# Kernel optimization log

Hardware: AMD Instinct MI355X
Metric: run time of the kernel (lower is better)

## Reference

```python
import jax, jax.numpy as jnp
import numpy as np

EPS = 1e-5
NUM_HEADS = 8

def _bn(x, w, b, m, v):
    # inference-mode BatchNorm2d over channel dim of (B,C,H,W)
    inv = w / jnp.sqrt(v + EPS)
    return x * inv[None, :, None, None] + (b - m * inv)[None, :, None, None]

def _conv1x1(x, W, b):
    # 1x1 conv == per-pixel matmul: W is (out_ch, in_ch)
    return jnp.einsum('bchw,ec->behw', x, W) + b[None, :, None, None]

def _forward(x, bn1_w, bn1_b, bn1_m, bn1_v, Wq, bq, Wk, bk, Wv, bv, gamma, temperature,
             conv_w, conv_b, cbn_w, cbn_b, cbn_m, cbn_v, rs_w, rs_b, rbn_w, rbn_b, rbn_m, rbn_v):
    B, C, Wd, Hd = x.shape
    S = Wd * Hd
    E = Wq.shape[0]
    hd = E // NUM_HEADS
    xa = jax.nn.relu(_bn(x, bn1_w, bn1_b, bn1_m, bn1_v))
    def proj(Wm, bm):
        return _conv1x1(xa, Wm, bm).reshape(B, NUM_HEADS, hd, S).transpose(0, 1, 3, 2)  # (B,h,S,d)
    q = proj(Wq, bq)
    k = proj(Wk, bk)
    v = proj(Wv, bv)
    scores = jnp.einsum('bhsd,bhtd->bhst', q, k) / temperature  # (B,h,S,S)
    scores = scores - jnp.max(scores, axis=-1, keepdims=True)   # redundant amax-subtract as in source
    attn = jax.nn.softmax(scores, axis=-1)
    out = jnp.einsum('bhst,bhtd->bhsd', attn, v)
    out = out.transpose(0, 1, 3, 2).reshape(B, E, Wd, Hd)
    conv_path = jax.nn.relu(_bn(_conv1x1(x, conv_w, conv_b), cbn_w, cbn_b, cbn_m, cbn_v))
    fused = gamma[0] * out + conv_path
    return jax.nn.gelu(_bn(_conv1x1(fused, rs_w, rs_b), rbn_w, rbn_b, rbn_m, rbn_v), approximate=False)

def setup_inputs() -> dict:
    key = jax.random.key(0)
    ks = jax.random.split(key, 18)
    C, E = 256, 512
    n = lambda k, s, sc=0.02: jax.random.normal(k, s, jnp.float32) * sc
    return {
        'x': jax.random.normal(ks[0], (1, C, 64, 64), jnp.float32),
        'bn1_w': 1.0 + n(ks[1], (C,), 0.1), 'bn1_b': n(ks[2], (C,), 0.1),
        'bn1_m': n(ks[3], (C,), 0.05), 'bn1_v': 0.5 + jax.random.uniform(ks[4], (C,), jnp.float32),
        'Wq': n(ks[5], (E, C)), 'bq': jnp.zeros((E,), jnp.float32),
        'Wk': n(ks[6], (E, C)), 'bk': jnp.zeros((E,), jnp.float32),
        'Wv': n(ks[7], (E, C)), 'bv': jnp.zeros((E,), jnp.float32),
        'gamma': jnp.full((1,), 0.5, jnp.float32),
        'temperature': jnp.asarray(0.85, jnp.float32),
        'conv_w': n(ks[8], (E, C)), 'conv_b': jnp.zeros((E,), jnp.float32),
        'cbn_w': 1.0 + n(ks[9], (E,), 0.1), 'cbn_b': n(ks[10], (E,), 0.1),
        'cbn_m': n(ks[11], (E,), 0.05), 'cbn_v': 0.5 + jax.random.uniform(ks[12], (E,), jnp.float32),
        'rs_w': n(ks[13], (C, E)), 'rs_b': jnp.zeros((C,), jnp.float32),
        'rbn_w': 1.0 + n(ks[14], (C,), 0.1), 'rbn_b': n(ks[15], (C,), 0.1),
        'rbn_m': n(ks[16], (C,), 0.05), 'rbn_v': 0.5 + jax.random.uniform(ks[17], (C,), jnp.float32),
    }

def reference(x, bn1_w, bn1_b, bn1_m, bn1_v, Wq, bq, Wk, bk, Wv, bv, gamma, temperature,
              conv_w, conv_b, cbn_w, cbn_b, cbn_m, cbn_v, rs_w, rs_b, rbn_w, rbn_b, rbn_m, rbn_v):
    return _forward(x, bn1_w, bn1_b, bn1_m, bn1_v, Wq, bq, Wk, bk, Wv, bv, gamma, temperature,
                    conv_w, conv_b, cbn_w, cbn_b, cbn_m, cbn_v, rs_w, rs_b, rbn_w, rbn_b, rbn_m, rbn_v)
```

## Files before the change

kernel.cpp:

```cpp
#include <hip/hip_runtime.h>

#define S_DIM 4096
#define C_IN  256
#define E_DIM 512
#define HD    64
#define EPSV  1e-5f

typedef __attribute__((ext_vector_type(8))) short s8v;
typedef __attribute__((ext_vector_type(4))) short s4v;
typedef __attribute__((ext_vector_type(4))) float f4v;
typedef __attribute__((ext_vector_type(16))) float f16v;

__device__ __forceinline__ float bf2f(unsigned short h){
  union{unsigned u; float f;} v; v.u = ((unsigned)h)<<16; return v.f;
}
__device__ __forceinline__ unsigned short f2bf(float f){
  union{float f; unsigned u;} v; v.f = f;
  unsigned r = v.u + 0x7fffu + ((v.u>>16)&1u);
  return (unsigned short)(r>>16);
}
__device__ __forceinline__ unsigned cvtpk_bf16(float lo, float hi_){
  unsigned r;
  asm("v_cvt_pk_bf16_f32 %0, %1, %2" : "=v"(r) : "v"(lo), "v"(hi_));
  return r;
}
__device__ __forceinline__ s8v lds_rd8(const unsigned short* b, int row, int ck){
  return *(const s8v*)&b[(row<<6) + (((ck)^(row&7))<<3)];
}
__device__ __forceinline__ s4v lds_rd4q(const unsigned short* b, int row, int q4){
  return *(const s4v*)&b[(row<<6) + (((q4)^(row&15))<<2)];
}
__device__ __forceinline__ int swz64(int col, int row){
  return (col & ~56) | ((((col>>3)&7) ^ (row&7))<<3);
}
__device__ __forceinline__ void gl_lds16(const unsigned short* g, unsigned short* l){
  __builtin_amdgcn_global_load_lds(
      (const __attribute__((address_space(1))) unsigned int*)g,
      (__attribute__((address_space(3))) unsigned int*)l, 16, 0, 0);
}

__global__ __launch_bounds__(256) void k_pre(const float* __restrict__ w0,
    const float* __restrict__ w1, const float* __restrict__ w2,
    const float* __restrict__ w3, const float* __restrict__ w4,
    unsigned short* __restrict__ dst,
    const float* __restrict__ x,
    const float* __restrict__ bw, const float* __restrict__ bb,
    const float* __restrict__ bm, const float* __restrict__ bvar,
    unsigned short* __restrict__ XaT, unsigned short* __restrict__ XrT){
  int fb = blockIdx.x;
  int tid = threadIdx.x;
  if(fb < 2560){
    int z = fb >> 9, i = (fb & 511)*256 + tid;
    const float* s = (z==0)?w0:(z==1)?w1:(z==2)?w2:(z==3)?w3:w4;
    float v = s[i];
    int idx;
    if(z < 4){
      int e = i>>8, c = i&255;
      idx = z*(E_DIM*C_IN) + e*C_IN + swz64(c, e);
    } else {
      int c = i>>9, e = i&511;
      idx = 4*(E_DIM*C_IN) + c*E_DIM + swz64(e, c);
    }
    dst[idx] = f2bf(v);
    return;
  }
  int b = fb - 2560;
  __shared__ float tile[32][33];
  int tx = tid & 31, ty = tid >> 5;
  int s0 = (b & 127)*32, c0 = (b >> 7)*32;
  #pragma unroll
  for(int p=0;p<4;p++){
    int c = c0 + ty + p*8;
    tile[ty+p*8][tx] = x[c*S_DIM + s0 + tx];
  }
  __syncthreads();
  int cc = c0 + tx;
  float inv  = bw[cc] * rsqrtf(bvar[cc] + EPSV);
  float beta = bb[cc] - bm[cc]*inv;
  #pragma unroll
  for(int p=0;p<4;p++){
    int s = s0 + ty + p*8;
    float v = tile[tx][ty+p*8];
    float a = v*inv + beta; a = a>0.f?a:0.f;
    int ccp = swz64(cc, s);
    XaT[s*C_IN + ccp] = f2bf(a);
    XrT[s*C_IN + ccp] = f2bf(v);
  }
}

__global__ __launch_bounds__(256) void k_proj(
    const unsigned short* __restrict__ XaT, const unsigned short* __restrict__ XrT,
    const unsigned short* __restrict__ Wb,
    const float* __restrict__ bq, const float* __restrict__ bk,
    const float* __restrict__ bvb, const float* __restrict__ bc,
    const float* __restrict__ cw, const float* __restrict__ cbb,
    const float* __restrict__ cm, const float* __restrict__ cvv,
    unsigned short* __restrict__ QT, unsigned short* __restrict__ KT,
    unsigned short* __restrict__ Vx, unsigned short* __restrict__ CT){
  int z = blockIdx.z;
  const unsigned short* Xin = (z==3) ? XrT : XaT;
  const unsigned short* W   = Wb + z*(E_DIM*C_IN);
  const float* bias = (z==0)?bq:(z==1)?bk:(z==2)?bvb:bc;

  __shared__ unsigned short Als[128*64];
  __shared__ unsigned short Bls[64*64];
  int tid = threadIdx.x;
  int w = tid>>6, l = tid&63, g = l>>4, c16 = l&15;
  int wr = w>>1, wc = w&1;
  int s0 = blockIdx.y*128, e0 = blockIdx.x*64;

  f4v acc[4][2];
  #pragma unroll
  for(int m=0;m<4;m++)
    #pragma unroll
    for(int n=0;n<2;n++) acc[m][n] = (f4v){0.f,0.f,0.f,0.f};

  for(int kk=0;kk<4;kk++){
    __syncthreads();
    #pragma unroll
    for(int p=0;p<4;p++){
      int flat = p*256 + tid, row = flat>>3, ch = flat&7;
      gl_lds16(&Xin[(s0+row)*C_IN + kk*64 + ch*8], Als + (p*256 + w*64)*8);
    }
    #pragma unroll
    for(int p=0;p<2;p++){
      int flat = p*256 + tid, row = flat>>3, ch = flat&7;
      gl_lds16(&W[(e0+row)*C_IN + kk*64 + ch*8], Bls + (p*256 + w*64)*8);
    }
    asm volatile("s_waitcnt vmcnt(0)" ::: "memory");
    __syncthreads();
    #pragma unroll
    for(int kb=0;kb<2;kb++){
      s8v bfr[2];
      #pragma unroll
      for(int n=0;n<2;n++) bfr[n] = lds_rd8(Bls, wc*32 + n*16 + c16, g + kb*4);
      #pragma unroll
      for(int m=0;m<4;m++){
        s8v af = lds_rd8(Als, wr*64 + m*16 + c16, g + kb*4);
        #pragma unroll
        for(int n=0;n<2;n++)
          acc[m][n] = __builtin_amdgcn_mfma_f32_16x16x32_bf16(af, bfr[n], acc[m][n], 0,0,0);
      }
    }
  }
  #pragma unroll
  for(int n=0;n<2;n++){
    int e = e0 + wc*32 + n*16 + c16;
    float bsv = bias[e];
    float cinv = 0.f, cbeta = 0.f;
    if(z==3){ cinv = cw[e]*rsqrtf(cvv[e]+EPSV); cbeta = cbb[e] - cm[e]*cinv; }
    #pragma unroll
    for(int m=0;m<4;m++){
      int sb = s0 + wr*64 + m*16 + g*4;
      if(z==2){
        s4v pk;
        #pragma unroll
        for(int i=0;i<4;i++) pk[i] = (short)f2bf(acc[m][n][i] + bsv);
        int sb2 = (sb & ~63) | ((((sb>>2)&15) ^ (e&15))<<2);
        *(s4v*)&Vx[e*S_DIM + sb2] = pk;
      } else {
        unsigned short* dst = (z==0)?QT:(z==1)?KT:CT;
        #pragma unroll
        for(int i=0;i<4;i++){
          float vv = acc[m][n][i] + bsv;
          if(z==3){ vv = vv*cinv + cbeta; vv = vv>0.f?vv:0.f; }
          int key = sb+i;
          int ee = e;
          if(z==1) ee = swz64(e, key);
          dst[key*E_DIM + ee] = f2bf(vv);
        }
      }
    }
  }
}

__global__ __launch_bounds__(512,2) void k_attn(
    const unsigned short* __restrict__ QT, const unsigned short* __restrict__ KT,
    const unsigned short* __restrict__ Vx, const unsigned short* __restrict__ CT,
    const float* __restrict__ gamma, const float* __restrict__ temp,
    unsigned short* __restrict__ fusedT){
  __shared__ unsigned short SM[65536];
  int tid = threadIdx.x;
  int w = tid>>6, l = tid&63, l31 = l&31, hi = l>>5;
  int qh = w>>2, kh = w&3;
  int bx = blockIdx.x;
  int h = bx&7;
  int q0b = (bx>>3)*128;
  float scl = 1.4426950408889634f / temp[0];

  #define STAGE(BUF, T) { \
    _Pragma("unroll") \
    for(int j=0;j<8;j++){ \
      int flat = (w*8+j)*64 + l; \
      int tile = flat>>9, gg = flat&511, row = gg>>3, ch = gg&7; \
      int khp = tile&3; \
      int sK = khp*1024 + (T)*64; \
      const unsigned short* src = (tile<4) \
        ? &KT[(sK+row)*E_DIM + h*HD + ch*8] \
        : &Vx[(h*HD+row)*S_DIM + sK + ch*8]; \
      gl_lds16(src, SM + (BUF)*32768 + (w*8+j)*512); \
    } }

  STAGE(0, 0);

  s8v qf[2][4];
  #pragma unroll
  for(int qg=0;qg<2;qg++){
    int q = q0b + qh*64 + qg*32 + l31;
    #pragma unroll
    for(int ks=0;ks<4;ks++){
      s8v r = *(const s8v*)&QT[q*E_DIM + h*HD + ks*16 + hi*8];
      #pragma unroll
      for(int j=0;j<8;j++) qf[qg][ks][j] = (short)f2bf(bf2f((unsigned short)r[j])*scl);
    }
  }

  f16v oacc[2][2];
  #pragma unroll
  for(int qg=0;qg<2;qg++)
    #pragma unroll
    for(int dt=0;dt<2;dt++)
      #pragma unroll
      for(int r=0;r<16;r++) oacc[qg][dt][r]=0.f;
  float lrun[2] = {0.f, 0.f};

  int buf = 0;
  #pragma unroll 1
  for(int t=0;t<16;t++){
    asm volatile("s_waitcnt vmcnt(0)" ::: "memory");
    __syncthreads();
    if(t<15) STAGE(buf^1, t+1);
    const unsigned short* Kb = SM + buf*32768 + kh*4096;
    const unsigned short* Vb = SM + buf*32768 + (4+kh)*4096;

    #pragma unroll
    for(int sub=0;sub<2;sub++){
      int kr = sub*32 + l31;
      s8v kf[4];
      #pragma unroll
      for(int ks=0;ks<4;ks++) kf[ks] = lds_rd8(Kb, kr, ks*2 + hi);

      union{ s8v v; unsigned u[4]; } pa[2][2];
      #pragma unroll
      for(int qg=0;qg<2;qg++){
        f16v d;
        #pragma unroll
        for(int r=0;r<16;r++) d[r]=0.f;
        __builtin_amdgcn_s_setprio(1);
        #pragma unroll
        for(int ks=0;ks<4;ks++)
          d = __builtin_amdgcn_mfma_f32_32x32x16_bf16(kf[ks], qf[qg][ks], d, 0,0,0);
        __builtin_amdgcn_s_setprio(0);
        float e_[16], ls = 0.f;
        #pragma unroll
        for(int r=0;r<16;r++){ e_[r] = __builtin_amdgcn_exp2f(d[r]); ls += e_[r]; }
        lrun[qg] += ls;
        #pragma unroll
        for(int j=0;j<4;j++){
          pa[qg][0].u[j] = cvtpk_bf16(e_[2*j],   e_[2*j+1]);
          pa[qg][1].u[j] = cvtpk_bf16(e_[8+2*j], e_[8+2*j+1]);
        }
      }
      __builtin_amdgcn_s_setprio(1);
      #pragma unroll
      for(int dt=0;dt<2;dt++){
        int vr = dt*32 + l31;
        union{ s8v v; s4v h2[2]; } vf;
        vf.h2[0] = lds_rd4q(Vb, vr, sub*8 + hi);
        vf.h2[1] = lds_rd4q(Vb, vr, sub*8 + 2 + hi);
        oacc[0][dt] = __builtin_amdgcn_mfma_f32_32x32x16_bf16(pa[0][0].v, vf.v, oacc[0][dt], 0,0,0);
        oacc[1][dt] = __builtin_amdgcn_mfma_f32_32x32x16_bf16(pa[1][0].v, vf.v, oacc[1][dt], 0,0,0);
        vf.h2[0] = lds_rd4q(Vb, vr, sub*8 + 4 + hi);
        vf.h2[1] = lds_rd4q(Vb, vr, sub*8 + 6 + hi);
        oacc[0][dt] = __builtin_amdgcn_mfma_f32_32x32x16_bf16(pa[0][1].v, vf.v, oacc[0][dt], 0,0,0);
        oacc[1][dt] = __builtin_amdgcn_mfma_f32_32x32x16_bf16(pa[1][1].v, vf.v, oacc[1][dt], 0,0,0);
      }
      __builtin_amdgcn_s_setprio(0);
    }
    buf ^= 1;
  }

  #pragma unroll
  for(int qg=0;qg<2;qg++) lrun[qg] += __shfl_xor(lrun[qg], 32);

  float* slab = (float*)SM;
  float* l_buf = slab + 6*64*33;
  float ga = gamma[0];
  #pragma unroll
  for(int qg=0;qg<2;qg++){
    __syncthreads();
    if(kh!=0){
      float* dst = slab + ((qh*3 + (kh-1))*64 + l)*33;
      #pragma unroll
      for(int r=0;r<16;r++){ dst[r] = oacc[qg][0][r]; dst[16+r] = oacc[qg][1][r]; }
      dst[32] = lrun[qg];
    }
    __syncthreads();
    if(kh==0){
      float lt = lrun[qg];
      #pragma unroll
      for(int s=0;s<3;s++){
        const float* src = slab + ((qh*3 + s)*64 + l)*33;
        #pragma unroll
        for(int r=0;r<16;r++){ oacc[qg][0][r] += src[r]; oacc[qg][1][r] += src[16+r]; }
        lt += src[32];
      }
      if(hi==0) l_buf[qh*32 + l31] = lt;
    }
    __syncthreads();
    if(kh==0){
      #pragma unroll
      for(int g4=0;g4<4;g4++){
        float4 lv = *(float4*)&l_buf[qh*32 + g4*8 + hi*4];
        float rl[4] = {ga/lv.x, ga/lv.y, ga/lv.z, ga/lv.w};
        #pragma unroll
        for(int dt=0;dt<2;dt++){
          int e = h*HD + dt*32 + l31;
          #pragma unroll
          for(int j=0;j<4;j++){
            int r = g4*4 + j;
            int qrow = q0b + qh*64 + qg*32 + j + g4*8 + hi*4;
            float o = oacc[qg][dt][r]*rl[j] + bf2f(CT[qrow*E_DIM + e]);
            fusedT[qrow*E_DIM + swz64(e, qrow)] = f2bf(o);
          }
        }
      }
    }
  }
  #undef STAGE
}

__global__ __launch_bounds__(256) void k_final(
    const unsigned short* __restrict__ Wrs,
    const unsigned short* __restrict__ fusedT,
    const float* __restrict__ rsb,
    const float* __restrict__ rw, const float* __restrict__ rbb,
    const float* __restrict__ rm, const float* __restrict__ rv,
    float* __restrict__ out){
  __shared__ unsigned short Als[64*64];
  __shared__ unsigned short Bls[64*64];
  int tid = threadIdx.x;
  int w = tid>>6, l = tid&63, g = l>>4, c16 = l&15;
  int wr2 = w>>1, wc2 = w&1;
  int sB0 = blockIdx.x*64, c0 = blockIdx.y*64;
  f4v acc[2][2];
  #pragma unroll
  for(int m=0;m<2;m++)
    #pragma unroll
    for(int n=0;n<2;n++) acc[m][n]=(f4v){0.f,0.f,0.f,0.f};
  for(int kk=0;kk<8;kk++){
    __syncthreads();
    #pragma unroll
    for(int p=0;p<2;p++){
      int flat = p*256+tid, row=flat>>3, ch=flat&7;
      gl_lds16(&Wrs[(c0+row)*E_DIM + kk*64 + ch*8], Als + (p*256 + w*64)*8);
    }
    #pragma unroll
    for(int p=0;p<2;p++){
      int flat = p*256+tid, row=flat>>3, ch=flat&7;
      gl_lds16(&fusedT[(sB0+row)*E_DIM + kk*64 + ch*8], Bls + (p*256 + w*64)*8);
    }
    asm volatile("s_waitcnt vmcnt(0)" ::: "memory");
    __syncthreads();
    #pragma unroll
    for(int kb=0;kb<2;kb++){
      s8v af[2]; s8v bfr[2];
      #pragma unroll
      for(int m=0;m<2;m++) af[m] = lds_rd8(Als, wr2*32 + m*16 + c16, g + kb*4);
      #pragma unroll
      for(int n=0;n<2;n++) bfr[n] = lds_rd8(Bls, wc2*32 + n*16 + c16, g + kb*4);
      #pragma unroll
      for(int m=0;m<2;m++)
        #pragma unroll
        for(int n=0;n<2;n++)
          acc[m][n] = __builtin_amdgcn_mfma_f32_16x16x32_bf16(af[m], bfr[n], acc[m][n],0,0,0);
    }
  }
  #pragma unroll
  for(int m=0;m<2;m++){
    #pragma unroll
    for(int i=0;i<4;i++){
      int c = c0 + wr2*32 + m*16 + g*4 + i;
      float bias = rsb[c];
      float rinv = rw[c]*rsqrtf(rv[c]+EPSV);
      float rbeta = rbb[c] - rm[c]*rinv;
      #pragma unroll
      for(int n=0;n<2;n++){
        int s = sB0 + wc2*32 + n*16 + c16;
        float vv = acc[m][n][i] + bias;
        vv = vv*rinv + rbeta;
        out[c*S_DIM + s] = 0.5f*vv*(1.0f + erff(vv*0.70710678118f));
      }
    }
  }
}

extern "C" void kernel_launch(void* const* d_in, const int* in_sizes, int n_in,
                              void* d_out, int out_size, void* d_ws, size_t ws_size,
                              hipStream_t stream){
  const float* x     = (const float*)d_in[0];
  const float* bn1w  = (const float*)d_in[1];
  const float* bn1b  = (const float*)d_in[2];
  const float* bn1m  = (const float*)d_in[3];
  const float* bn1v  = (const float*)d_in[4];
  const float* Wq    = (const float*)d_in[5];
  const float* bq    = (const float*)d_in[6];
  const float* Wk    = (const float*)d_in[7];
  const float* bk    = (const float*)d_in[8];
  const float* Wv    = (const float*)d_in[9];
  const float* bv    = (const float*)d_in[10];
  const float* gamma = (const float*)d_in[11];
  const float* temp  = (const float*)d_in[12];
  const float* convw = (const float*)d_in[13];
  const float* convb = (const float*)d_in[14];
  const float* cbnw  = (const float*)d_in[15];
  const float* cbnb  = (const float*)d_in[16];
  const float* cbnm  = (const float*)d_in[17];
  const float* cbnv  = (const float*)d_in[18];
  const float* rsw   = (const float*)d_in[19];
  const float* rsbp  = (const float*)d_in[20];
  const float* rbnw  = (const float*)d_in[21];
  const float* rbnb  = (const float*)d_in[22];
  const float* rbnm  = (const float*)d_in[23];
  const float* rbnv  = (const float*)d_in[24];
  float* out = (float*)d_out;

  unsigned short* ws  = (unsigned short*)d_ws;
  unsigned short* XaT = ws;
  unsigned short* XrT = XaT + S_DIM*C_IN;
  unsigned short* Wb  = XrT + S_DIM*C_IN;
  unsigned short* Wrs = Wb + 4*E_DIM*C_IN;
  unsigned short* QT  = Wrs + C_IN*E_DIM;
  unsigned short* KT  = QT + S_DIM*E_DIM;
  unsigned short* Vx  = KT + S_DIM*E_DIM;
  unsigned short* CT  = Vx + S_DIM*E_DIM;
  unsigned short* fusedT = CT + S_DIM*E_DIM;

  k_pre<<<dim3(3584),256,0,stream>>>(Wq, Wk, Wv, convw, rsw, Wb,
                                     x, bn1w, bn1b, bn1m, bn1v, XaT, XrT);
  k_proj<<<dim3(8,32,4),256,0,stream>>>(XaT, XrT, Wb, bq, bk, bv, convb,
                                        cbnw, cbnb, cbnm, cbnv, QT, KT, Vx, CT);
  k_attn<<<dim3(256),512,0,stream>>>(QT, KT, Vx, CT, gamma, temp, fusedT);
  k_final<<<dim3(64,4),256,0,stream>>>(Wrs, fusedT, rsbp, rbnw, rbnb, rbnm, rbnv, out);
}
```

Before: 77.61 us.

## Halve attention query and key tiles to fit two blocks per CU

Measured after the change: 82.54 us. 1.06x slower.

```diff
diff --git a/kernel.cpp b/kernel.cpp
--- a/kernel.cpp
+++ b/kernel.cpp
@@ -27,8 +27,8 @@
 __device__ __forceinline__ s8v lds_rd8(const unsigned short* b, int row, int ck){
   return *(const s8v*)&b[(row<<6) + (((ck)^(row&7))<<3)];
 }
-__device__ __forceinline__ s4v lds_rd4q(const unsigned short* b, int row, int q4){
-  return *(const s4v*)&b[(row<<6) + (((q4)^(row&15))<<2)];
+__device__ __forceinline__ s4v lds_rd4v(const unsigned short* b, int row, int q4){
+  return *(const s4v*)&b[(row<<5) + (((q4) ^ ((row>>1)&7))<<2)];
 }
 __device__ __forceinline__ int swz64(int col, int row){
   return (col & ~56) | ((((col>>3)&7) ^ (row&7))<<3);
@@ -156,7 +156,7 @@
         s4v pk;
         #pragma unroll
         for(int i=0;i<4;i++) pk[i] = (short)f2bf(acc[m][n][i] + bsv);
-        int sb2 = (sb & ~63) | ((((sb>>2)&15) ^ (e&15))<<2);
+        int sb2 = (sb & ~31) | ((((sb>>2)&7) ^ ((e>>1)&7))<<2);
         *(s4v*)&Vx[e*S_DIM + sb2] = pk;
       } else {
         unsigned short* dst = (z==0)?QT:(z==1)?KT:CT;
@@ -179,150 +179,137 @@
     const unsigned short* __restrict__ Vx, const unsigned short* __restrict__ CT,
     const float* __restrict__ gamma, const float* __restrict__ temp,
     unsigned short* __restrict__ fusedT){
-  __shared__ unsigned short SM[65536];
+  __shared__ unsigned short SM[32768];
   int tid = threadIdx.x;
   int w = tid>>6, l = tid&63, l31 = l&31, hi = l>>5;
   int qh = w>>2, kh = w&3;
   int bx = blockIdx.x;
   int h = bx&7;
-  int q0b = (bx>>3)*128;
+  int q0b = (bx>>3)*64;
   float scl = 1.4426950408889634f / temp[0];
 
   #define STAGE(BUF, T) { \
     _Pragma("unroll") \
-    for(int j=0;j<8;j++){ \
-      int flat = (w*8+j)*64 + l; \
-      int tile = flat>>9, gg = flat&511, row = gg>>3, ch = gg&7; \
+    for(int j=0;j<4;j++){ \
+      int flat = (w*4+j)*64 + l; \
+      int tile = flat>>8, gg = flat&255; \
       int khp = tile&3; \
-      int sK = khp*1024 + (T)*64; \
-      const unsigned short* src = (tile<4) \
-        ? &KT[(sK+row)*E_DIM + h*HD + ch*8] \
-        : &Vx[(h*HD+row)*S_DIM + sK + ch*8]; \
-      gl_lds16(src, SM + (BUF)*32768 + (w*8+j)*512); \
+      int sK = khp*1024 + (T)*32; \
+      const unsigned short* src; \
+      if(tile<4){ int row = gg>>3, ch = gg&7; \
+        src = &KT[(sK+row)*E_DIM + h*HD + ch*8]; \
+      } else { int row = gg>>2, ch = gg&3; \
+        src = &Vx[(h*HD+row)*S_DIM + sK + ch*8]; \
+      } \
+      gl_lds16(src, SM + (BUF)*16384 + (w*4+j)*512); \
     } }
 
   STAGE(0, 0);
 
-  s8v qf[2][4];
-  #pragma unroll
-  for(int qg=0;qg<2;qg++){
-    int q = q0b + qh*64 + qg*32 + l31;
+  s8v qf[4];
+  {
+    int q = q0b + qh*32 + l31;
     #pragma unroll
     for(int ks=0;ks<4;ks++){
       s8v r = *(const s8v*)&QT[q*E_DIM + h*HD + ks*16 + hi*8];
       #pragma unroll
-      for(int j=0;j<8;j++) qf[qg][ks][j] = (short)f2bf(bf2f((unsigned short)r[j])*scl);
-    }
-  }
-
-  f16v oacc[2][2];
-  #pragma unroll
-  for(int qg=0;qg<2;qg++)
-    #pragma unroll
-    for(int dt=0;dt<2;dt++)
-      #pragma unroll
-      for(int r=0;r<16;r++) oacc[qg][dt][r]=0.f;
-  float lrun[2] = {0.f, 0.f};
+      for(int j=0;j<8;j++) qf[ks][j] = (short)f2bf(bf2f((unsigned short)r[j])*scl);
+    }
+  }
+
+  f16v oacc[2];
+  #pragma unroll
+  for(int dt=0;dt<2;dt++)
+    #pragma unroll
+    for(int r=0;r<16;r++) oacc[dt][r]=0.f;
+  float lrun = 0.f;
 
   int buf = 0;
   #pragma unroll 1
-  for(int t=0;t<16;t++){
+  for(int t=0;t<32;t++){
     asm volatile("s_waitcnt vmcnt(0)" ::: "memory");
     __syncthreads();
-    if(t<15) STAGE(buf^1, t+1);
-    const unsigned short* Kb = SM + buf*32768 + kh*4096;
-    const unsigned short* Vb = SM + buf*32768 + (4+kh)*4096;
-
-    #pragma unroll
-    for(int sub=0;sub<2;sub++){
-      int kr = sub*32 + l31;
-      s8v kf[4];
-      #pragma unroll
-      for(int ks=0;ks<4;ks++) kf[ks] = lds_rd8(Kb, kr, ks*2 + hi);
-
-      union{ s8v v; unsigned u[4]; } pa[2][2];
-      #pragma unroll
-      for(int qg=0;qg<2;qg++){
-        f16v d;
-        #pragma unroll
-        for(int r=0;r<16;r++) d[r]=0.f;
-        __builtin_amdgcn_s_setprio(1);
-        #pragma unroll
-        for(int ks=0;ks<4;ks++)
-          d = __builtin_amdgcn_mfma_f32_32x32x16_bf16(kf[ks], qf[qg][ks], d, 0,0,0);
-        __builtin_amdgcn_s_setprio(0);
-        float e_[16], ls = 0.f;
-        #pragma unroll
-        for(int r=0;r<16;r++){ e_[r] = __builtin_amdgcn_exp2f(d[r]); ls += e_[r]; }
-        lrun[qg] += ls;
-        #pragma unroll
-        for(int j=0;j<4;j++){
-          pa[qg][0].u[j] = cvtpk_bf16(e_[2*j],   e_[2*j+1]);
-          pa[qg][1].u[j] = cvtpk_bf16(e_[8+2*j], e_[8+2*j+1]);
-        }
-      }
-      __builtin_amdgcn_s_setprio(1);
-      #pragma unroll
-      for(int dt=0;dt<2;dt++){
-        int vr = dt*32 + l31;
-        union{ s8v v; s4v h2[2]; } vf;
-        vf.h2[0] = lds_rd4q(Vb, vr, sub*8 + hi);
-        vf.h2[1] = lds_rd4q(Vb, vr, sub*8 + 2 + hi);
-        oacc[0][dt] = __builtin_amdgcn_mfma_f32_32x32x16_bf16(pa[0][0].v, vf.v, oacc[0][dt], 0,0,0);
-        oacc[1][dt] = __builtin_amdgcn_mfma_f32_32x32x16_bf16(pa[1][0].v, vf.v, oacc[1][dt], 0,0,0);
-        vf.h2[0] = lds_rd4q(Vb, vr, sub*8 + 4 + hi);
-        vf.h2[1] = lds_rd4q(Vb, vr, sub*8 + 6 + hi);
-        oacc[0][dt] = __builtin_amdgcn_mfma_f32_32x32x16_bf16(pa[0][1].v, vf.v, oacc[0][dt], 0,0,0);
-        oacc[1][dt] = __builtin_amdgcn_mfma_f32_32x32x16_bf16(pa[1][1].v, vf.v, oacc[1][dt], 0,0,0);
-      }
-      __builtin_amdgcn_s_setprio(0);
-    }
+    if(t<31) STAGE(buf^1, t+1);
+    const unsigned short* Kb = SM + buf*16384 + kh*2048;
+    const unsigned short* Vb = SM + buf*16384 + (4+kh)*2048;
+
+    s8v kf[4];
+    #pragma unroll
+    for(int ks=0;ks<4;ks++) kf[ks] = lds_rd8(Kb, l31, ks*2 + hi);
+
+    f16v d;
+    #pragma unroll
+    for(int r=0;r<16;r++) d[r]=0.f;
+    __builtin_amdgcn_s_setprio(1);
+    #pragma unroll
+    for(int ks=0;ks<4;ks++)
+      d = __builtin_amdgcn_mfma_f32_32x32x16_bf16(kf[ks], qf[ks], d, 0,0,0);
+    __builtin_amdgcn_s_setprio(0);
+    float e_[16], ls = 0.f;
+    #pragma unroll
+    for(int r=0;r<16;r++){ e_[r] = __builtin_amdgcn_exp2f(d[r]); ls += e_[r]; }
+    lrun += ls;
+    union{ s8v v; unsigned u[4]; } pa0, pa1;
+    #pragma unroll
+    for(int j=0;j<4;j++){
+      pa0.u[j] = cvtpk_bf16(e_[2*j],   e_[2*j+1]);
+      pa1.u[j] = cvtpk_bf16(e_[8+2*j], e_[8+2*j+1]);
+    }
+    __builtin_amdgcn_s_setprio(1);
+    #pragma unroll
+    for(int dt=0;dt<2;dt++){
+      int vr = dt*32 + l31;
+      union{ s8v v; s4v h2[2]; } vf;
+      vf.h2[0] = lds_rd4v(Vb, vr, hi);
+      vf.h2[1] = lds_rd4v(Vb, vr, 2 + hi);
+      oacc[dt] = __builtin_amdgcn_mfma_f32_32x32x16_bf16(pa0.v, vf.v, oacc[dt], 0,0,0);
+      vf.h2[0] = lds_rd4v(Vb, vr, 4 + hi);
+      vf.h2[1] = lds_rd4v(Vb, vr, 6 + hi);
+      oacc[dt] = __builtin_amdgcn_mfma_f32_32x32x16_bf16(pa1.v, vf.v, oacc[dt], 0,0,0);
+    }
+    __builtin_amdgcn_s_setprio(0);
     buf ^= 1;
   }
 
-  #pragma unroll
-  for(int qg=0;qg<2;qg++) lrun[qg] += __shfl_xor(lrun[qg], 32);
+  lrun += __shfl_xor(lrun, 32);
 
   float* slab = (float*)SM;
   float* l_buf = slab + 6*64*33;
   float ga = gamma[0];
-  #pragma unroll
-  for(int qg=0;qg<2;qg++){
-    __syncthreads();
-    if(kh!=0){
-      float* dst = slab + ((qh*3 + (kh-1))*64 + l)*33;
-      #pragma unroll
-      for(int r=0;r<16;r++){ dst[r] = oacc[qg][0][r]; dst[16+r] = oacc[qg][1][r]; }
-      dst[32] = lrun[qg];
-    }
-    __syncthreads();
-    if(kh==0){
-      float lt = lrun[qg];
-      #pragma unroll
-      for(int s=0;s<3;s++){
-        const float* src = slab + ((qh*3 + s)*64 + l)*33;
+  __syncthreads();
+  if(kh!=0){
+    float* dst = slab + ((qh*3 + (kh-1))*64 + l)*33;
+    #pragma unroll
+    for(int r=0;r<16;r++){ dst[r] = oacc[0][r]; dst[16+r] = oacc[1][r]; }
+    dst[32] = lrun;
+  }
+  __syncthreads();
+  if(kh==0){
+    float lt = lrun;
+    #pragma unroll
+    for(int s=0;s<3;s++){
+      const float* src = slab + ((qh*3 + s)*64 + l)*33;
+      #pragma unroll
+      for(int r=0;r<16;r++){ oacc[0][r] += src[r]; oacc[1][r] += src[16+r]; }
+      lt += src[32];
+    }
+    if(hi==0) l_buf[qh*32 + l31] = lt;
+  }
+  __syncthreads();
+  if(kh==0){
+    #pragma unroll
+    for(int g4=0;g4<4;g4++){
+      float4 lv = *(float4*)&l_buf[qh*32 + g4*8 + hi*4];
+      float rl[4] = {ga/lv.x, ga/lv.y, ga/lv.z, ga/lv.w};
+      #pragma unroll
+      for(int dt=0;dt<2;dt++){
+        int e = h*HD + dt*32 + l31;
         #pragma unroll
-        for(int r=0;r<16;r++){ oacc[qg][0][r] += src[r]; oacc[qg][1][r] += src[16+r]; }
-        lt += src[32];
-      }
-      if(hi==0) l_buf[qh*32 + l31] = lt;
-    }
-    __syncthreads();
-    if(kh==0){
-      #pragma unroll
-      for(int g4=0;g4<4;g4++){
-        float4 lv = *(float4*)&l_buf[qh*32 + g4*8 + hi*4];
-        float rl[4] = {ga/lv.x, ga/lv.y, ga/lv.z, ga/lv.w};
-        #pragma unroll
-        for(int dt=0;dt<2;dt++){
-          int e = h*HD + dt*32 + l31;
-          #pragma unroll
-          for(int j=0;j<4;j++){
-            int r = g4*4 + j;
-            int qrow = q0b + qh*64 + qg*32 + j + g4*8 + hi*4;
-            float o = oacc[qg][dt][r]*rl[j] + bf2f(CT[qrow*E_DIM + e]);
-            fusedT[qrow*E_DIM + swz64(e, qrow)] = f2bf(o);
-          }
+        for(int j=0;j<4;j++){
+          int r = g4*4 + j;
+          int qrow = q0b + qh*32 + j + g4*8 + hi*4;
+          float o = oacc[dt][r]*rl[j] + bf2f(CT[qrow*E_DIM + e]);
+          fusedT[qrow*E_DIM + swz64(e, qrow)] = f2bf(o);
         }
       }
     }
@@ -440,6 +427,6 @@
                                      x, bn1w, bn1b, bn1m, bn1v, XaT, XrT);
   k_proj<<<dim3(8,32,4),256,0,stream>>>(XaT, XrT, Wb, bq, bk, bv, convb,
                                         cbnw, cbnb, cbnm, cbnv, QT, KT, Vx, CT);
-  k_attn<<<dim3(256),512,0,stream>>>(QT, KT, Vx, CT, gamma, temp, fusedT);
+  k_attn<<<dim3(512),512,0,stream>>>(QT, KT, Vx, CT, gamma, temp, fusedT);
   k_final<<<dim3(64,4),256,0,stream>>>(Wrs, fusedT, rsbp, rbnw, rbnb, rbnm, rbnv, out);
 }
```
